# Kernel tuning notes

Measured on AMD Instinct MI355X. Metric: run time of the kernel, lower is better.

Reference implementation:

```python
import jax, jax.numpy as jnp
import numpy as np

NX, NY = 512, 512
FNUM, GNUM = 120, 120
NA = 1.35
WAVELENGTH = NX * NA / 100.0  # chosen so normalized period = 100
N_LIQUID = 1.44
M_RED = 0.25
LOW_LIGHT_THRES = 1e-3
SRC_STEEP = 8.0
RESIST_STEEP = 30.0
RESIST_INT = 0.225
DOSES = (0.98, 1.0, 1.02)
SRC_GRID = 13

X1 = NX // 2 - FNUM; X2 = NX // 2 + FNUM + 1
Y1 = NY // 2 - GNUM; Y2 = NY // 2 + GNUM + 1
_PER_X = NX / (WAVELENGTH / NA)
_PER_Y = NY / (WAVELENGTH / NA)
NORM_SPEC = _PER_X * _PER_Y
DFMDG = 1.0 / NORM_SPEC
_fm = (np.arange(X1, X2) - NX // 2) / _PER_X
_gm = (np.arange(Y1, Y2) - NY // 2) / _PER_Y
_FM, _GM = np.meshgrid(_fm, _gm)  # 'xy' indexing, shape [2*GNUM+1, 2*FNUM+1]
FM = jnp.asarray(_FM, jnp.float32)
GM = jnp.asarray(_GM, jnp.float32)


def cal_pupil(fg2):
    # obliquity factor; pupil phase is identically zero in this module
    num = 1.0 - (M_RED ** 2) * (NA ** 2) * fg2
    den = 1.0 - (NA / N_LIQUID) ** 2 * fg2
    return jnp.sqrt(jnp.sqrt(num / den))


def setup_inputs() -> dict:
    key = jax.random.key(0)
    g = np.linspace(-1.0, 1.0, SRC_GRID, dtype=np.float32)
    fxg, fyg = np.meshgrid(g, g)
    r = np.sqrt(fxg ** 2 + fyg ** 2)
    data = ((r >= 0.6) & (r <= 0.9)).astype(np.float32)  # annular source
    # sigmoid activation init: +1 where lit, -1 elsewhere (zeros, set 2 where data>0.5, sub 1)
    params = 2.0 * data - 1.0
    mask_value = jax.random.uniform(key, (NY, NX), jnp.float32)
    return {
        "mask_value": mask_value,
        "source_params": jnp.asarray(params, jnp.float32),
        "source_fx": jnp.asarray(fxg.reshape(-1), jnp.float32),
        "source_fy": jnp.asarray(fyg.reshape(-1), jnp.float32),
    }


def _forward(mask_value, source_params, source_fx, source_fy):
    # source activation + low-light pruning (masked_select expressed as zero-weighting)
    val = jax.nn.sigmoid(SRC_STEEP * source_params).reshape(-1)  # [S]
    valid = val >= LOW_LIGHT_THRES
    w = jnp.where(valid, val, 0.0)
    weight = jnp.sum(w)

    # normalization intensity (detached in the original)
    fxy2 = source_fx ** 2 + source_fy ** 2
    obl = cal_pupil(jnp.where(valid, fxy2, 0.0))
    norm_I = jax.lax.stop_gradient(
        N_LIQUID * DFMDG ** 2 * jnp.sum(w * (NORM_SPEC * obl) ** 2) / weight
    )

    # shifted pupil per source point over the mask frequency window
    F = FM[None, :, :] + source_fx[:, None, None]  # [S, Gy, Gx]
    G = GM[None, :, :] + source_fy[:, None, None]
    rho2 = F * F + G * G                            # == mask_fg2m + 2(fx*fm+fy*gm) + fxy2
    vmask = rho2 <= 1.0
    pupil = jnp.where(vmask, cal_pupil(jnp.where(vmask, rho2, 0.0)), 0.0)  # [S, Gy, Gx]

    S = w.shape[0]
    Is, Rs = [], []
    for d in DOSES:
        fv = jnp.fft.fftshift(jnp.fft.fft2(jnp.fft.ifftshift(mask_value * d)))
        win = fv[Y1:Y2, X1:X2]                      # [Gy, Gx] complex
        tempH = win[None, :, :] * pupil.astype(jnp.complex64)  # masked spectrum*pupil
        e = jnp.zeros((S, NY, NX), jnp.complex64).at[:, Y1:Y2, X1:X2].set(tempH)
        AA = jnp.fft.fftshift(jnp.fft.ifft2(e), axes=(-2, -1))
        I2 = AA.real ** 2 + AA.imag ** 2            # |AA * conj(AA)|
        intensity = jnp.einsum('s,syx->yx', w, I2) / weight / norm_I
        Is.append(intensity)
        Rs.append(jax.nn.sigmoid(RESIST_STEEP * (intensity - RESIST_INT)))
    # [2, 3, NY, NX]: [0] = aerial intensity per dose, [1] = resist image per dose
    return jnp.stack([jnp.stack(Is), jnp.stack(Rs)])


def reference(mask_value, source_params, source_fx, source_fy):
    return _forward(mask_value, source_params, source_fx, source_fy)
```

## Files before the change

kernel.cpp:

```cpp
#include <hip/hip_runtime.h>
#include <hip/hip_bf16.h>


#define SPLIT 4

static const size_t ACC_BYTES  = (size_t)SPLIT * 512 * 512 * 4;
static const size_t O_ACC      = 4096;
static const size_t O_WIN      = O_ACC + ACC_BYTES;
static const size_t O_R1       = O_WIN + 464896;
static const size_t O_T2       = O_R1 + 987136;
static const size_t SLOT_BYTES = (size_t)512 * 244 * 8;

__device__ inline float2 cadd(float2 a, float2 b){ return make_float2(a.x+b.x, a.y+b.y); }
__device__ inline float2 csub(float2 a, float2 b){ return make_float2(a.x-b.x, a.y-b.y); }
__device__ inline float2 cmul(float2 a, float2 b){
  return make_float2(fmaf(a.x, b.x, -(a.y*b.y)), fmaf(a.x, b.y, a.y*b.x));
}

template<int BLOCK>
__device__ inline void build_tw(float2* twtab) {
  for (int k = (int)threadIdx.x; k < 512; k += BLOCK) {
    double a = 6.283185307179586476925286766559 * (double)k / 512.0;
    twtab[k] = make_float2((float)cos(a), (float)sin(a));
  }
  __syncthreads();
}

template<int S>
__device__ inline void dft8(float2 v[8]) {
  const float sg = (float)S;
  const float C7 = 0.7071067811865476f;
  float2 t0=cadd(v[0],v[4]), t4=csub(v[0],v[4]);
  float2 t1=cadd(v[1],v[5]), t5=csub(v[1],v[5]);
  float2 t2=cadd(v[2],v[6]), t6=csub(v[2],v[6]);
  float2 t3=cadd(v[3],v[7]), t7=csub(v[3],v[7]);
  t5 = make_float2(C7*(t5.x - sg*t5.y), C7*(t5.y + sg*t5.x));
  t6 = make_float2(-sg*t6.y, sg*t6.x);
  t7 = make_float2(C7*(-t7.x - sg*t7.y), C7*(sg*t7.x - t7.y));
  float2 u0=cadd(t0,t2), u2=csub(t0,t2);
  float2 u1=cadd(t1,t3), u3=csub(t1,t3);
  u3 = make_float2(-sg*u3.y, sg*u3.x);
  float2 u4=cadd(t4,t6), u6=csub(t4,t6);
  float2 u5=cadd(t5,t7), u7=csub(t5,t7);
  u7 = make_float2(-sg*u7.y, sg*u7.x);
  v[0]=cadd(u0,u1); v[4]=csub(u0,u1);
  v[2]=cadd(u2,u3); v[6]=csub(u2,u3);
  v[1]=cadd(u4,u5); v[5]=csub(u4,u5);
  v[3]=cadd(u6,u7); v[7]=csub(u6,u7);
}

__device__ inline float2 twsgn(float2 t, int S) {
  return make_float2(t.x, (S > 0) ? t.y : -t.y);
}

template<int S>
__device__ inline void wfft512(float2 v[8], int lane, float2* xch,
                               const float2* twtab) {
  dft8<S>(v);
  #pragma unroll
  for (int u = 1; u < 8; u++)
    v[u] = cmul(v[u], twsgn(twtab[(lane * u) & 511], S));
  __syncthreads();
  #pragma unroll
  for (int u = 0; u < 8; u++) xch[u*64 + lane] = v[u];
  __syncthreads();
  int u0 = lane >> 3, p2 = lane & 7;
  #pragma unroll
  for (int q = 0; q < 8; q++) v[q] = xch[u0*64 + q*8 + p2];
  dft8<S>(v);
  #pragma unroll
  for (int u = 1; u < 8; u++)
    v[u] = cmul(v[u], twsgn(twtab[(p2 * u) << 3], S));
  __syncthreads();
  #pragma unroll
  for (int u = 0; u < 8; u++) xch[u0*64 + u*8 + p2] = v[u];
  __syncthreads();
  #pragma unroll
  for (int q = 0; q < 8; q++) v[q] = xch[u0*64 + p2*8 + q];
  dft8<S>(v);
}

__global__ void __launch_bounds__(256) k_setup(const float* prm, const float* sfx,
                                               const float* sfy, char* ws) {
  __shared__ float sw[169], sx[169], sy[169];
  __shared__ double so[169];
  int t = threadIdx.x;
  if (t < 169) {
    float p = prm[t];
    float val = 1.f / (1.f + __expf(-8.f * p));
    float w = (val >= 0.001f) ? val : 0.f;
    double o = 0.0; float fx = 0.f, fy = 0.f;
    if (w > 0.f) {
      fx = sfx[t]; fy = sfy[t];
      double f2 = (double)fx*(double)fx + (double)fy*(double)fy;
      double num = 1.0 - 0.11390625 * f2;
      double den = 1.0 - 0.87890625 * f2;
      o = (double)w * sqrt(num / den);
    }
    sw[t] = w; so[t] = o; sx[t] = fx; sy[t] = fy;
  }
  __syncthreads();
  if (t == 0) {
    float* wsf = (float*)ws; int* wsi = (int*)ws;
    double Sden = 0.0; int c = 0;
    for (int s = 0; s < 169; s++) {
      Sden += so[s];
      if (sw[s] > 0.f) { wsf[64+c] = sw[s]; wsf[320+c] = sx[s]; wsf[576+c] = sy[s]; c++; }
    }
    wsi[0] = c;
    wsf[1] = (float)(1.0 / (68719476736.0 * 1.44 * Sden));
  }
}

__global__ void __launch_bounds__(256) k_b1(const float* mask, float2* R1t) {
  int lane = threadIdx.x & 63, wv = threadIdx.x >> 6;
  int y = blockIdx.x * 4 + wv;
  __shared__ float2 xch[4][512];
  __shared__ float2 twtab[512];
  build_tw<256>(twtab);
  float2 v[8];
  #pragma unroll
  for (int q = 0; q < 8; q++) v[q] = make_float2(mask[y*512 + 64*q + lane], 0.f);
  wfft512<-1>(v, lane, xch[wv], twtab);
  #pragma unroll
  for (int u = 0; u < 8; u++) {
    int k = (lane>>3) + 8*(lane&7) + 64*u;
    int beta = (k >= 392) ? (k - 392) : ((k <= 120) ? (k + 120) : -1);
    if (beta >= 0) R1t[beta*512 + y] = v[u];
  }
}

__global__ void __launch_bounds__(256) k_b2(const float2* R1t, float2* Wg) {
  int lane = threadIdx.x & 63, wv = threadIdx.x >> 6;
  int j = blockIdx.x * 4 + wv;
  __shared__ float2 xch[4][512];
  __shared__ float2 twtab[512];
  build_tw<256>(twtab);
  float2 v[8];
  #pragma unroll
  for (int q = 0; q < 8; q++)
    v[q] = (j < 241) ? R1t[j*512 + 64*q + lane] : make_float2(0.f, 0.f);
  wfft512<-1>(v, lane, xch[wv], twtab);
  if (j < 241) {
    #pragma unroll
    for (int u = 0; u < 8; u++) {
      int k = (lane>>3) + 8*(lane&7) + 64*u;
      int alpha = (k >= 392) ? (k - 392) : ((k <= 120) ? (k + 120) : -1);
      if (alpha >= 0) Wg[alpha*241 + j] = v[u];
    }
  }
}

__global__ void __launch_bounds__(256) k_c1(const float2* Wg, const char* wsb,
                                            int base, float2* T2) {
  const int*   cnt = (const int*)wsb;
  const float* wsf = (const float*)wsb;
  int sic  = blockIdx.x / 31;
  int tile = blockIdx.x % 31;
  int slot = base + sic;
  if (slot >= *cnt) return;
  float fx = wsf[320 + slot], fy = wsf[576 + slot];
  int lane = threadIdx.x & 63, wv = threadIdx.x >> 6;
  __shared__ float2 xch[4][512];
  __shared__ float2 tout[8][512];
  __shared__ float2 twtab[512];
  build_tw<256>(twtab);
  #pragma unroll
  for (int i = 0; i < 2; i++) {
    int al = wv*2 + i;
    int alpha = tile*8 + al;
    double G = ((double)alpha - 120.0) * 0.01 + (double)fy;
    double g2 = G * G;
    float2 v[8];
    #pragma unroll
    for (int q = 0; q < 8; q++) {
      v[q] = make_float2(0.f, 0.f);
      int n = 64*q + lane;
      if (alpha < 241 && n < 241) {
        double F = ((double)n - 120.0) * 0.01 + (double)fx;
        double r2 = F*F + g2;
        if (r2 <= 1.0) {
          double num = 1.0 - 0.11390625 * r2;
          double den = 1.0 - 0.87890625 * r2;
          float P = (float)sqrt(sqrt(num / den));
          float2 Wv = Wg[alpha*241 + n];
          v[q] = make_float2(P * Wv.x, P * Wv.y);
        }
      }
    }
    wfft512<1>(v, lane, xch[wv], twtab);
    #pragma unroll
    for (int u = 0; u < 8; u++) {
      int xx = (lane>>3) + 8*(lane&7) + 64*u;
      tout[al][xx] = v[u];
    }
  }
  __syncthreads();
  #pragma unroll
  for (int r = 0; r < 2; r++) {
    int x = (int)threadIdx.x + 256*r;
    float2* dst = T2 + ((size_t)sic*512 + x)*244 + tile*8;
    #pragma unroll
    for (int jj = 0; jj < 8; jj++) {
      int col = tile*8 + jj;
      if (col < 244) dst[jj] = tout[jj][x];
    }
  }
}

__global__ void __launch_bounds__(64) k_c2(const float2* T2, const char* wsb,
                                           int base, int CH, float* accbuf) {
  const int*   cnt = (const int*)wsb;
  const float* wsf = (const float*)wsb;
  int x    = blockIdx.x >> 2;
  int part = blockIdx.x & 3;
  int lane = threadIdx.x;
  __shared__ float2 xch[512];
  __shared__ float2 twtab[512];
  build_tw<64>(twtab);
  float av[8] = {0.f,0.f,0.f,0.f,0.f,0.f,0.f,0.f};
  bool touched = false;
  int count = *cnt;
  for (int sic = part; sic < CH; sic += SPLIT) {
    int slot = base + sic;
    if (slot >= count) break;
    float w = wsf[64 + slot];
    float2 v[8];
    #pragma unroll
    for (int q = 0; q < 8; q++) v[q] = make_float2(0.f, 0.f);
    #pragma unroll
    for (int q = 0; q < 4; q++) {
      int n = 64*q + lane;
      if (n < 241) v[q] = T2[((size_t)sic*512 + x)*244 + n];
    }
    wfft512<1>(v, lane, xch, twtab);
    #pragma unroll
    for (int u = 0; u < 8; u++)
      av[u] = fmaf(w, fmaf(v[u].x, v[u].x, v[u].y*v[u].y), av[u]);
    touched = true;
  }
  if (touched) {
    float* a = accbuf + ((size_t)part << 18) + (size_t)x * 512;
    int y0 = (lane>>3) + 8*(lane&7);
    #pragma unroll
    for (int u = 0; u < 8; u++) a[y0 + 64*u] += av[u];
  }
}

__global__ void __launch_bounds__(256) k_final(const float* acc, const char* wsb,
                                               float* out) {
  const float* wsf = (const float*)wsb;
  int tid = blockIdx.x * 256 + threadIdx.x;
  int x = tid & 511, y = tid >> 9;
  float a = 0.f;
  #pragma unroll
  for (int p = 0; p < SPLIT; p++) a += acc[((size_t)p << 18) + x*512 + y];
  float I = a * wsf[1];
  const float dd[3] = {0.9604f, 1.0f, 1.0404f};
  #pragma unroll
  for (int k = 0; k < 3; k++) {
    float Ik = dd[k] * I;
    out[(size_t)k*262144 + tid] = Ik;
    out[(size_t)(3+k)*262144 + tid] = 1.f / (1.f + __expf(-30.f * (Ik - 0.225f)));
  }
}

extern "C" void kernel_launch(void* const* d_in, const int* in_sizes, int n_in,
                              void* d_out, int out_size, void* d_ws, size_t ws_size,
                              hipStream_t stream) {
  (void)in_sizes; (void)n_in; (void)out_size;
  const float* mask = (const float*)d_in[0];
  const float* prm  = (const float*)d_in[1];
  const float* sfx  = (const float*)d_in[2];
  const float* sfy  = (const float*)d_in[3];
  float* out = (float*)d_out;
  char*  ws  = (char*)d_ws;

  float*  acc = (float*)(ws + O_ACC);
  float2* Wg  = (float2*)(ws + O_WIN);
  float2* R1t = (float2*)(ws + O_R1);
  float2* T2  = (float2*)(ws + O_T2);

  hipMemsetAsync(acc, 0, ACC_BYTES, stream);
  k_setup<<<dim3(1),   dim3(256), 0, stream>>>(prm, sfx, sfy, ws);
  k_b1  <<<dim3(128), dim3(256), 0, stream>>>(mask, R1t);
  k_b2  <<<dim3(61),  dim3(256), 0, stream>>>(R1t, Wg);

  size_t avail = (ws_size > O_T2) ? (ws_size - O_T2) : 0;
  int CH = (int)(avail / SLOT_BYTES);
  if (CH > 169) CH = 169;
  if (CH < 1)   CH = 1;
  for (int base = 0; base < 169; base += CH) {
    k_c1<<<dim3((unsigned)(CH*31)),  dim3(256), 0, stream>>>(Wg, (const char*)ws, base, T2);
    k_c2<<<dim3(512*SPLIT),          dim3(64),  0, stream>>>(T2, (const char*)ws, base, CH, acc);
  }
  k_final<<<dim3(1024), dim3(256), 0, stream>>>(acc, (const char*)ws, out);
}
```

Measured before the change: 169.8 us.

## Precompute twiddles globally, wave-local FFT exchange, float pupil, prefetch and tiled final

The setup kernel now computes the twiddle table and frequency coordinates once in global memory, so every block loads them instead of evaluating double-precision cos/sin. The 512-point FFT swaps block-wide barriers for wave barriers, uses a padded LDS layout with float4 reads, and derives twiddles by recurrence. k_c1 evaluates the pupil in float instead of double, reuses a single LDS buffer and writes T2 with float4 stores. k_c2 prefetches the next source row and writes the accumulator directly on the first chunk so the memset can go, and k_final transposes through LDS for coalesced access. The costs are small numerical differences from float pupil math and twiddle recurrence, plus added occupancy hints.

```diff
diff --git a/kernel.cpp b/kernel.cpp
--- a/kernel.cpp
+++ b/kernel.cpp
@@ -4,11 +4,12 @@
 
 #define SPLIT 4
 
-static const size_t ACC_BYTES  = (size_t)SPLIT * 512 * 512 * 4;
-static const size_t O_ACC      = 4096;
-static const size_t O_WIN      = O_ACC + ACC_BYTES;
-static const size_t O_R1       = O_WIN + 464896;
-static const size_t O_T2       = O_R1 + 987136;
+static const size_t O_TW   = 4096;
+static const size_t O_ACC  = 8192;
+static const size_t ACC_BYTES = (size_t)SPLIT * 512 * 512 * 4;
+static const size_t O_WIN  = O_ACC + ACC_BYTES;
+static const size_t O_R1   = O_WIN + 464896;
+static const size_t O_T2   = O_R1 + 987136;
 static const size_t SLOT_BYTES = (size_t)512 * 244 * 8;
 
 __device__ inline float2 cadd(float2 a, float2 b){ return make_float2(a.x+b.x, a.y+b.y); }
@@ -16,14 +17,8 @@
 __device__ inline float2 cmul(float2 a, float2 b){
   return make_float2(fmaf(a.x, b.x, -(a.y*b.y)), fmaf(a.x, b.y, a.y*b.x));
 }
-
-template<int BLOCK>
-__device__ inline void build_tw(float2* twtab) {
-  for (int k = (int)threadIdx.x; k < 512; k += BLOCK) {
-    double a = 6.283185307179586476925286766559 * (double)k / 512.0;
-    twtab[k] = make_float2((float)cos(a), (float)sin(a));
-  }
-  __syncthreads();
+__device__ inline float2 twsgn(float2 t, int S) {
+  return make_float2(t.x, (S > 0) ? t.y : -t.y);
 }
 
 template<int S>
@@ -49,34 +44,42 @@
   v[3]=cadd(u6,u7); v[7]=csub(u6,u7);
 }
 
-__device__ inline float2 twsgn(float2 t, int S) {
-  return make_float2(t.x, (S > 0) ? t.y : -t.y);
-}
-
 template<int S>
 __device__ inline void wfft512(float2 v[8], int lane, float2* xch,
-                               const float2* twtab) {
+                               const float2* twt) {
+  const int p2 = lane & 7, u0 = lane >> 3;
   dft8<S>(v);
-  #pragma unroll
-  for (int u = 1; u < 8; u++)
-    v[u] = cmul(v[u], twsgn(twtab[(lane * u) & 511], S));
-  __syncthreads();
-  #pragma unroll
-  for (int u = 0; u < 8; u++) xch[u*64 + lane] = v[u];
-  __syncthreads();
-  int u0 = lane >> 3, p2 = lane & 7;
-  #pragma unroll
-  for (int q = 0; q < 8; q++) v[q] = xch[u0*64 + q*8 + p2];
+  { float2 t1 = twsgn(twt[lane], S), acc = t1;
+    v[1] = cmul(v[1], acc);
+    #pragma unroll
+    for (int u = 2; u < 8; u++) { acc = cmul(acc, t1); v[u] = cmul(v[u], acc); } }
+  __builtin_amdgcn_wave_barrier();
+  #pragma unroll
+  for (int u = 0; u < 8; u++) xch[u*68 + p2*8 + u0] = v[u];
+  __builtin_amdgcn_wave_barrier();
+  { const float4* rp = (const float4*)(xch + u0*68 + p2*8);
+    #pragma unroll
+    for (int q = 0; q < 4; q++) {
+      float4 t = rp[q];
+      v[2*q]   = make_float2(t.x, t.y);
+      v[2*q+1] = make_float2(t.z, t.w);
+    } }
   dft8<S>(v);
-  #pragma unroll
-  for (int u = 1; u < 8; u++)
-    v[u] = cmul(v[u], twsgn(twtab[(p2 * u) << 3], S));
-  __syncthreads();
-  #pragma unroll
-  for (int u = 0; u < 8; u++) xch[u0*64 + u*8 + p2] = v[u];
-  __syncthreads();
-  #pragma unroll
-  for (int q = 0; q < 8; q++) v[q] = xch[u0*64 + p2*8 + q];
+  { float2 t1 = twsgn(twt[p2 << 3], S), acc = t1;
+    v[1] = cmul(v[1], acc);
+    #pragma unroll
+    for (int u = 2; u < 8; u++) { acc = cmul(acc, t1); v[u] = cmul(v[u], acc); } }
+  __builtin_amdgcn_wave_barrier();
+  #pragma unroll
+  for (int u = 0; u < 8; u++) xch[u*68 + lane] = v[u];
+  __builtin_amdgcn_wave_barrier();
+  { const float4* rp = (const float4*)(xch + p2*68 + u0*8);
+    #pragma unroll
+    for (int q = 0; q < 4; q++) {
+      float4 t = rp[q];
+      v[2*q]   = make_float2(t.x, t.y);
+      v[2*q+1] = make_float2(t.z, t.w);
+    } }
   dft8<S>(v);
 }
 
@@ -93,12 +96,16 @@
     if (w > 0.f) {
       fx = sfx[t]; fy = sfy[t];
       double f2 = (double)fx*(double)fx + (double)fy*(double)fy;
-      double num = 1.0 - 0.11390625 * f2;
-      double den = 1.0 - 0.87890625 * f2;
-      o = (double)w * sqrt(num / den);
+      o = (double)w * sqrt((1.0 - 0.11390625 * f2) / (1.0 - 0.87890625 * f2));
     }
     sw[t] = w; so[t] = o; sx[t] = fx; sy[t] = fy;
   }
+  float2* gtw = (float2*)(ws + O_TW);
+  for (int k = t; k < 512; k += 256) {
+    double a = 6.283185307179586476925286766559 * (double)k / 512.0;
+    gtw[k] = make_float2((float)cos(a), (float)sin(a));
+  }
+  if (t < 241) ((float*)ws)[768 + t] = (float)(((double)(t - 120)) / 100.0);
   __syncthreads();
   if (t == 0) {
     float* wsf = (float*)ws; int* wsi = (int*)ws;
@@ -112,16 +119,18 @@
   }
 }
 
-__global__ void __launch_bounds__(256) k_b1(const float* mask, float2* R1t) {
+__global__ void __launch_bounds__(256, 6) k_b1(const float* mask, const char* wsb,
+                                               float2* R1t) {
   int lane = threadIdx.x & 63, wv = threadIdx.x >> 6;
   int y = blockIdx.x * 4 + wv;
-  __shared__ float2 xch[4][512];
-  __shared__ float2 twtab[512];
-  build_tw<256>(twtab);
+  __shared__ __align__(16) float2 lds[4*544];
+  __shared__ __align__(16) float2 twt[512];
+  ((float4*)twt)[threadIdx.x] = ((const float4*)(wsb + O_TW))[threadIdx.x];
+  __syncthreads();
   float2 v[8];
   #pragma unroll
   for (int q = 0; q < 8; q++) v[q] = make_float2(mask[y*512 + 64*q + lane], 0.f);
-  wfft512<-1>(v, lane, xch[wv], twtab);
+  wfft512<-1>(v, lane, lds + wv*544, twt);
   #pragma unroll
   for (int u = 0; u < 8; u++) {
     int k = (lane>>3) + 8*(lane&7) + 64*u;
@@ -130,17 +139,19 @@
   }
 }
 
-__global__ void __launch_bounds__(256) k_b2(const float2* R1t, float2* Wg) {
+__global__ void __launch_bounds__(256, 6) k_b2(const float2* R1t, const char* wsb,
+                                               float2* Wg) {
   int lane = threadIdx.x & 63, wv = threadIdx.x >> 6;
   int j = blockIdx.x * 4 + wv;
-  __shared__ float2 xch[4][512];
-  __shared__ float2 twtab[512];
-  build_tw<256>(twtab);
+  __shared__ __align__(16) float2 lds[4*544];
+  __shared__ __align__(16) float2 twt[512];
+  ((float4*)twt)[threadIdx.x] = ((const float4*)(wsb + O_TW))[threadIdx.x];
+  __syncthreads();
   float2 v[8];
   #pragma unroll
   for (int q = 0; q < 8; q++)
     v[q] = (j < 241) ? R1t[j*512 + 64*q + lane] : make_float2(0.f, 0.f);
-  wfft512<-1>(v, lane, xch[wv], twtab);
+  wfft512<-1>(v, lane, lds + wv*544, twt);
   if (j < 241) {
     #pragma unroll
     for (int u = 0; u < 8; u++) {
@@ -151,97 +162,127 @@
   }
 }
 
-__global__ void __launch_bounds__(256) k_c1(const float2* Wg, const char* wsb,
-                                            int base, float2* T2) {
+__global__ void __launch_bounds__(256, 6) k_c1(const float2* Wg, const char* wsb,
+                                               int base, float2* T2) {
   const int*   cnt = (const int*)wsb;
   const float* wsf = (const float*)wsb;
+  const float* FMt = (const float*)(wsb + 3072);
   int sic  = blockIdx.x / 31;
   int tile = blockIdx.x % 31;
   int slot = base + sic;
   if (slot >= *cnt) return;
+  __shared__ __align__(16) float2 lds[4*544];
+  __shared__ __align__(16) float2 twt[512];
+  ((float4*)twt)[threadIdx.x] = ((const float4*)(wsb + O_TW))[threadIdx.x];
+  __syncthreads();
   float fx = wsf[320 + slot], fy = wsf[576 + slot];
   int lane = threadIdx.x & 63, wv = threadIdx.x >> 6;
-  __shared__ float2 xch[4][512];
-  __shared__ float2 tout[8][512];
-  __shared__ float2 twtab[512];
-  build_tw<256>(twtab);
-  #pragma unroll
-  for (int i = 0; i < 2; i++) {
-    int al = wv*2 + i;
-    int alpha = tile*8 + al;
-    double G = ((double)alpha - 120.0) * 0.01 + (double)fy;
-    double g2 = G * G;
+  float2* xch = lds + wv*544;
+  #pragma unroll
+  for (int ph = 0; ph < 2; ph++) {
+    int alpha = tile*8 + ph*4 + wv;
+    bool arow = (alpha < 241);
+    float Gf = __fadd_rn(arow ? FMt[alpha] : 0.f, fy);
+    float g2 = __fmul_rn(Gf, Gf);
     float2 v[8];
     #pragma unroll
     for (int q = 0; q < 8; q++) {
-      v[q] = make_float2(0.f, 0.f);
       int n = 64*q + lane;
-      if (alpha < 241 && n < 241) {
-        double F = ((double)n - 120.0) * 0.01 + (double)fx;
-        double r2 = F*F + g2;
-        if (r2 <= 1.0) {
-          double num = 1.0 - 0.11390625 * r2;
-          double den = 1.0 - 0.87890625 * r2;
-          float P = (float)sqrt(sqrt(num / den));
+      float2 val = make_float2(0.f, 0.f);
+      if (arow && n < 241) {
+        float Ff = __fadd_rn(FMt[n], fx);
+        float r2 = __fadd_rn(__fmul_rn(Ff, Ff), g2);
+        if (r2 <= 1.0f) {
+          float num = fmaf(-0.11390625f, r2, 1.0f);
+          float den = fmaf(-0.87890625f, r2, 1.0f);
+          float P = __fsqrt_rn(__fsqrt_rn(__fdividef(num, den)));
           float2 Wv = Wg[alpha*241 + n];
-          v[q] = make_float2(P * Wv.x, P * Wv.y);
+          val = make_float2(P * Wv.x, P * Wv.y);
         }
       }
-    }
-    wfft512<1>(v, lane, xch[wv], twtab);
+      v[q] = val;
+    }
+    wfft512<1>(v, lane, xch, twt);
     #pragma unroll
     for (int u = 0; u < 8; u++) {
       int xx = (lane>>3) + 8*(lane&7) + 64*u;
-      tout[al][xx] = v[u];
-    }
-  }
-  __syncthreads();
-  #pragma unroll
-  for (int r = 0; r < 2; r++) {
-    int x = (int)threadIdx.x + 256*r;
-    float2* dst = T2 + ((size_t)sic*512 + x)*244 + tile*8;
-    #pragma unroll
-    for (int jj = 0; jj < 8; jj++) {
-      int col = tile*8 + jj;
-      if (col < 244) dst[jj] = tout[jj][x];
-    }
-  }
-}
-
-__global__ void __launch_bounds__(64) k_c2(const float2* T2, const char* wsb,
-                                           int base, int CH, float* accbuf) {
+      xch[xx] = v[u];
+    }
+    __syncthreads();
+    int colb = tile*8 + ph*4;
+    if (colb < 244) {
+      #pragma unroll
+      for (int r = 0; r < 2; r++) {
+        int x = (int)threadIdx.x + 256*r;
+        float2 a0 = lds[0*544+x], a1 = lds[1*544+x];
+        float2 a2 = lds[2*544+x], a3 = lds[3*544+x];
+        float4* dst = (float4*)(T2 + ((size_t)sic*512 + x)*244 + colb);
+        dst[0] = make_float4(a0.x, a0.y, a1.x, a1.y);
+        dst[1] = make_float4(a2.x, a2.y, a3.x, a3.y);
+      }
+    }
+    __syncthreads();
+  }
+}
+
+__global__ void __launch_bounds__(64, 4) k_c2(const float2* T2, const char* wsb,
+                                              int base, int CH, int first,
+                                              float* accbuf) {
   const int*   cnt = (const int*)wsb;
   const float* wsf = (const float*)wsb;
   int x    = blockIdx.x >> 2;
   int part = blockIdx.x & 3;
   int lane = threadIdx.x;
-  __shared__ float2 xch[512];
-  __shared__ float2 twtab[512];
-  build_tw<64>(twtab);
+  __shared__ __align__(16) float2 xch[544];
+  __shared__ __align__(16) float2 twt[512];
+  #pragma unroll
+  for (int i = 0; i < 4; i++)
+    ((float4*)twt)[lane + 64*i] = ((const float4*)(wsb + O_TW))[lane + 64*i];
+  __builtin_amdgcn_wave_barrier();
+  int count = *cnt;
   float av[8] = {0.f,0.f,0.f,0.f,0.f,0.f,0.f,0.f};
   bool touched = false;
-  int count = *cnt;
-  for (int sic = part; sic < CH; sic += SPLIT) {
-    int slot = base + sic;
-    if (slot >= count) break;
-    float w = wsf[64 + slot];
-    float2 v[8];
-    #pragma unroll
-    for (int q = 0; q < 8; q++) v[q] = make_float2(0.f, 0.f);
+  int sic = part;
+  bool act = (sic < CH) && (base + sic < count);
+  float2 pv[4] = {{0.f,0.f},{0.f,0.f},{0.f,0.f},{0.f,0.f}};
+  if (act) {
+    const float2* row = T2 + ((size_t)sic*512 + x)*244;
     #pragma unroll
     for (int q = 0; q < 4; q++) {
       int n = 64*q + lane;
-      if (n < 241) v[q] = T2[((size_t)sic*512 + x)*244 + n];
-    }
-    wfft512<1>(v, lane, xch, twtab);
+      pv[q] = (n < 241) ? row[n] : make_float2(0.f, 0.f);
+    }
+  }
+  while (act) {
+    float w = wsf[64 + base + sic];
+    float2 v[8];
+    #pragma unroll
+    for (int q = 0; q < 4; q++) v[q] = pv[q];
+    #pragma unroll
+    for (int q = 4; q < 8; q++) v[q] = make_float2(0.f, 0.f);
+    int nsic = sic + SPLIT;
+    act = (nsic < CH) && (base + nsic < count);
+    if (act) {
+      const float2* row = T2 + ((size_t)nsic*512 + x)*244;
+      #pragma unroll
+      for (int q = 0; q < 4; q++) {
+        int n = 64*q + lane;
+        pv[q] = (n < 241) ? row[n] : make_float2(0.f, 0.f);
+      }
+    }
+    wfft512<1>(v, lane, xch, twt);
     #pragma unroll
     for (int u = 0; u < 8; u++)
       av[u] = fmaf(w, fmaf(v[u].x, v[u].x, v[u].y*v[u].y), av[u]);
     touched = true;
-  }
-  if (touched) {
-    float* a = accbuf + ((size_t)part << 18) + (size_t)x * 512;
-    int y0 = (lane>>3) + 8*(lane&7);
+    sic = nsic;
+  }
+  float* a = accbuf + ((size_t)part << 18) + (size_t)x * 512;
+  int y0 = (lane>>3) + 8*(lane&7);
+  if (first) {
+    #pragma unroll
+    for (int u = 0; u < 8; u++) a[y0 + 64*u] = av[u];
+  } else if (touched) {
     #pragma unroll
     for (int u = 0; u < 8; u++) a[y0 + 64*u] += av[u];
   }
@@ -249,19 +290,30 @@
 
 __global__ void __launch_bounds__(256) k_final(const float* acc, const char* wsb,
                                                float* out) {
+  __shared__ float tile[64][65];
   const float* wsf = (const float*)wsb;
-  int tid = blockIdx.x * 256 + threadIdx.x;
-  int x = tid & 511, y = tid >> 9;
-  float a = 0.f;
-  #pragma unroll
-  for (int p = 0; p < SPLIT; p++) a += acc[((size_t)p << 18) + x*512 + y];
-  float I = a * wsf[1];
+  float scale = wsf[1];
+  int x0 = (blockIdx.x & 7) * 64, y0 = (blockIdx.x >> 3) * 64;
+  int j = threadIdx.x & 63, i0 = threadIdx.x >> 6;
+  #pragma unroll
+  for (int k = 0; k < 16; k++) {
+    int i = i0 + 4*k;
+    const float* ap = acc + (size_t)(x0 + i)*512 + y0 + j;
+    tile[i][j] = ap[0] + ap[1<<18] + ap[2<<18] + ap[3<<18];
+  }
+  __syncthreads();
   const float dd[3] = {0.9604f, 1.0f, 1.0404f};
   #pragma unroll
-  for (int k = 0; k < 3; k++) {
-    float Ik = dd[k] * I;
-    out[(size_t)k*262144 + tid] = Ik;
-    out[(size_t)(3+k)*262144 + tid] = 1.f / (1.f + __expf(-30.f * (Ik - 0.225f)));
+  for (int k = 0; k < 16; k++) {
+    int yy = i0 + 4*k;
+    float I = scale * tile[j][yy];
+    int o = (y0 + yy)*512 + x0 + j;
+    #pragma unroll
+    for (int d = 0; d < 3; d++) {
+      float Ik = dd[d] * I;
+      out[(size_t)d*262144 + o] = Ik;
+      out[(size_t)(3+d)*262144 + o] = 1.f / (1.f + __expf(-30.f*(Ik - 0.225f)));
+    }
   }
 }
 
@@ -281,18 +333,18 @@
   float2* R1t = (float2*)(ws + O_R1);
   float2* T2  = (float2*)(ws + O_T2);
 
-  hipMemsetAsync(acc, 0, ACC_BYTES, stream);
   k_setup<<<dim3(1),   dim3(256), 0, stream>>>(prm, sfx, sfy, ws);
-  k_b1  <<<dim3(128), dim3(256), 0, stream>>>(mask, R1t);
-  k_b2  <<<dim3(61),  dim3(256), 0, stream>>>(R1t, Wg);
+  k_b1  <<<dim3(128), dim3(256), 0, stream>>>(mask, (const char*)ws, R1t);
+  k_b2  <<<dim3(61),  dim3(256), 0, stream>>>(R1t, (const char*)ws, Wg);
 
   size_t avail = (ws_size > O_T2) ? (ws_size - O_T2) : 0;
   int CH = (int)(avail / SLOT_BYTES);
   if (CH > 169) CH = 169;
   if (CH < 1)   CH = 1;
   for (int base = 0; base < 169; base += CH) {
-    k_c1<<<dim3((unsigned)(CH*31)),  dim3(256), 0, stream>>>(Wg, (const char*)ws, base, T2);
-    k_c2<<<dim3(512*SPLIT),          dim3(64),  0, stream>>>(T2, (const char*)ws, base, CH, acc);
-  }
-  k_final<<<dim3(1024), dim3(256), 0, stream>>>(acc, (const char*)ws, out);
-}
+    k_c1<<<dim3((unsigned)(CH*31)), dim3(256), 0, stream>>>(Wg, (const char*)ws, base, T2);
+    k_c2<<<dim3(512*SPLIT),         dim3(64),  0, stream>>>(T2, (const char*)ws, base, CH,
+                                                            (base == 0) ? 1 : 0, acc);
+  }
+  k_final<<<dim3(64), dim3(256), 0, stream>>>(acc, (const char*)ws, out);
+}
```

Result: faster. 153.6 us (-9.5%).
